# Kernel tuning notes

Hardware: AMD Instinct MI355X
Metric: run time of the kernel (lower is better)

The kernel has to match this reference:

```python
import jax, jax.numpy as jnp
import numpy as np

D = 1024
HEADS = 16
HEAD_DIM = D // HEADS
B = 4
L = 1024


def setup_inputs() -> dict:
    key = jax.random.key(0)
    kq, kk, kv, kw, kb = jax.random.split(key, 5)
    Q = jax.random.normal(kq, (B, L, D), dtype=jnp.float32)
    K = jax.random.normal(kk, (B, L, D), dtype=jnp.float32)
    V = jax.random.normal(kv, (B, L, D), dtype=jnp.float32)
    # Output projection H: torch nn.Linear(D, D) -> weight (D, D), bias (D,)
    lim = 1.0 / np.sqrt(D)
    W_H = jax.random.uniform(kw, (D, D), minval=-lim, maxval=lim, dtype=jnp.float32)
    b_H = jax.random.uniform(kb, (D,), minval=-lim, maxval=lim, dtype=jnp.float32)
    mask = 0  # falsy -> no masking branch, matching `if mask` in the source
    return {"Q": Q, "K": K, "V": V, "W_H": W_H, "b_H": b_H, "mask": mask}


def reference(Q, K, V, W_H, b_H, mask):
    batch, q_len, _ = Q.shape
    k_len = K.shape[1]
    Qh = Q.reshape(batch, q_len, HEADS, HEAD_DIM)
    Kh = K.reshape(batch, k_len, HEADS, HEAD_DIM)
    Vh = V.reshape(batch, k_len, HEADS, HEAD_DIM)
    scores = jnp.einsum('bqhd,bkhd->bhqk', Qh, Kh)  # [B,H,Lq,Lk]
    if mask:  # mask is a Python scalar (0 -> skip), as in source
        scores = jnp.where(mask == 0, -jnp.inf, scores)
    # NOTE: source scales by sqrt(D), not sqrt(head_dim)
    attn = jax.nn.softmax(scores / np.sqrt(D).astype(np.float32), axis=3)
    out = jnp.einsum('bhql,blhd->bqhd', attn, Vh).reshape(batch, q_len, D)
    return out @ W_H.T + b_H
```

## Files before the change

kernel.cpp:

```cpp
#include <hip/hip_runtime.h>
#include <hip/hip_bf16.h>

typedef __attribute__((ext_vector_type(4))) float f32x4;
typedef __attribute__((ext_vector_type(8))) short bf16x8;

constexpr int Bn  = 4;
constexpr int Ln  = 1024;
constexpr int Dn  = 1024;
constexpr int Hn  = 16;
constexpr int HDn = 64;

static __device__ __forceinline__ unsigned short bf16r(float f) {
    union { float f; unsigned int u; } x;
    x.f = f;
    unsigned int r = x.u + 0x7fffu + ((x.u >> 16) & 1u);
    return (unsigned short)(r >> 16);
}

__global__ __launch_bounds__(256) void prep_kernel(
    const float* __restrict__ Kg, const float* __restrict__ Vg,
    const float* __restrict__ Wg, unsigned short* __restrict__ Kbf,
    unsigned short* __restrict__ Vtg, unsigned short* __restrict__ Wbf)
{
    const int tid = threadIdx.x;
    if (blockIdx.z == 4) {
        const int r0 = blockIdx.x * 64, c0 = blockIdx.y * 64;
        for (int i = 0; i < 4; ++i) {
            int e4 = i * 256 + tid;
            int r = e4 >> 4, c4 = e4 & 15;
            const float* p = Wg + (size_t)(r0 + r) * Dn + c0 + c4 * 4;
            float4 v = *(const float4*)p;
            ushort4 o;
            o.x = bf16r(v.x); o.y = bf16r(v.y); o.z = bf16r(v.z); o.w = bf16r(v.w);
            *(ushort4*)(Wbf + (size_t)(r0 + r) * Dn + c0 + c4 * 4) = o;
        }
        return;
    }

    __shared__ unsigned short T[64][72];
    const int k0 = blockIdx.x * 64;
    const int h  = blockIdx.y;
    const int b  = blockIdx.z;
    const float* Kb = Kg + (size_t)b * Ln * Dn + h * HDn;
    const float* Vb = Vg + (size_t)b * Ln * Dn + h * HDn;
    unsigned short* Ko = Kbf + (size_t)b * Ln * Dn + h * HDn;

    for (int i = 0; i < 4; ++i) {
        int e4 = i * 256 + tid;
        int r = e4 >> 4, c4 = e4 & 15;
        float4 kv = *(const float4*)(Kb + (size_t)(k0 + r) * Dn + c4 * 4);
        ushort4 o;
        o.x = bf16r(kv.x); o.y = bf16r(kv.y); o.z = bf16r(kv.z); o.w = bf16r(kv.w);
        *(ushort4*)(Ko + (size_t)(k0 + r) * Dn + c4 * 4) = o;
        float4 vv = *(const float4*)(Vb + (size_t)(k0 + r) * Dn + c4 * 4);
        T[c4 * 4 + 0][r] = bf16r(vv.x);
        T[c4 * 4 + 1][r] = bf16r(vv.y);
        T[c4 * 4 + 2][r] = bf16r(vv.z);
        T[c4 * 4 + 3][r] = bf16r(vv.w);
    }
    __syncthreads();
    unsigned short* out = Vtg + ((size_t)(b * Hn + h) * HDn) * Ln + k0;
    for (int i = 0; i < 2; ++i) {
        int e8 = i * 256 + tid;
        int r = e8 >> 3, c8 = e8 & 7;
        *(uint4*)(out + (size_t)r * Ln + c8 * 8) = *(const uint4*)&T[r][c8 * 8];
    }
}

__global__ __launch_bounds__(512) void attn_kernel(
    const float* __restrict__ Qg, const unsigned short* __restrict__ Kbf,
    const unsigned short* __restrict__ Vtg, unsigned short* __restrict__ Xg)
{
    __shared__ unsigned short Ks[64][72];
    __shared__ unsigned short Vts[64][72];
    __shared__ unsigned short Ps[128][72];

    const int tid  = threadIdx.x;
    const int wave = tid >> 6;
    const int lane = tid & 63;
    const int l16  = lane & 15;
    const int quad = lane >> 4;

    const int q0 = blockIdx.x * 128;
    const int h  = blockIdx.y;
    const int b  = blockIdx.z;

    const unsigned short* Kb16 = Kbf + (size_t)b * Ln * Dn + h * HDn;
    const unsigned short* Vtb  = Vtg + ((size_t)(b * Hn + h) * HDn) * Ln;

    bf16x8 aq0, aq1;
    {
        const float* qp = Qg + ((size_t)b * Ln + q0 + wave * 16 + l16) * Dn
                             + h * HDn + quad * 8;
        float4 a0 = *(const float4*)qp;
        float4 a1 = *(const float4*)(qp + 4);
        float4 a2 = *(const float4*)(qp + 32);
        float4 a3 = *(const float4*)(qp + 36);
        aq0[0] = (short)bf16r(a0.x); aq0[1] = (short)bf16r(a0.y);
        aq0[2] = (short)bf16r(a0.z); aq0[3] = (short)bf16r(a0.w);
        aq0[4] = (short)bf16r(a1.x); aq0[5] = (short)bf16r(a1.y);
        aq0[6] = (short)bf16r(a1.z); aq0[7] = (short)bf16r(a1.w);
        aq1[0] = (short)bf16r(a2.x); aq1[1] = (short)bf16r(a2.y);
        aq1[2] = (short)bf16r(a2.z); aq1[3] = (short)bf16r(a2.w);
        aq1[4] = (short)bf16r(a3.x); aq1[5] = (short)bf16r(a3.y);
        aq1[6] = (short)bf16r(a3.z); aq1[7] = (short)bf16r(a3.w);
    }

    const float SC = 1.4426950408889634f / 32.0f;

    float lsum[4] = {0.f, 0.f, 0.f, 0.f};
    f32x4 Oacc[4];
    for (int d = 0; d < 4; ++d) Oacc[d] = (f32x4){0.f, 0.f, 0.f, 0.f};

    for (int it = 0; it < Ln / 64; ++it) {
        const int k0 = it * 64;
        __syncthreads();
        {
            int r = tid >> 3, c8 = tid & 7;
            *(uint4*)&Ks[r][c8 * 8] =
                *(const uint4*)(Kb16 + (size_t)(k0 + r) * Dn + c8 * 8);
            *(uint4*)&Vts[r][c8 * 8] =
                *(const uint4*)(Vtb + (size_t)r * Ln + k0 + c8 * 8);
        }
        __syncthreads();

        f32x4 s[4];
        for (int n = 0; n < 4; ++n) {
            bf16x8 b0 = *(const bf16x8*)&Ks[n * 16 + l16][quad * 8];
            bf16x8 b1 = *(const bf16x8*)&Ks[n * 16 + l16][32 + quad * 8];
            f32x4 acc = (f32x4){0.f, 0.f, 0.f, 0.f};
            acc = __builtin_amdgcn_mfma_f32_16x16x32_bf16(aq0, b0, acc, 0, 0, 0);
            acc = __builtin_amdgcn_mfma_f32_16x16x32_bf16(aq1, b1, acc, 0, 0, 0);
            s[n] = acc;
        }

        for (int n = 0; n < 4; ++n)
            for (int r = 0; r < 4; ++r) {
                float p = exp2f(s[n][r] * SC);
                s[n][r] = p;
                lsum[r] += p;
            }

        for (int n = 0; n < 4; ++n)
            for (int r = 0; r < 4; ++r)
                Ps[wave * 16 + quad * 4 + r][n * 16 + l16] = bf16r(s[n][r]);

        for (int kk = 0; kk < 2; ++kk) {
            bf16x8 ap = *(const bf16x8*)&Ps[wave * 16 + l16][kk * 32 + quad * 8];
            for (int d = 0; d < 4; ++d) {
                bf16x8 bv = *(const bf16x8*)&Vts[d * 16 + l16][kk * 32 + quad * 8];
                Oacc[d] = __builtin_amdgcn_mfma_f32_16x16x32_bf16(ap, bv, Oacc[d], 0, 0, 0);
            }
        }
    }

    float linv[4];
    for (int r = 0; r < 4; ++r) {
        float rs = lsum[r];
        rs += __shfl_xor(rs, 1, 64);
        rs += __shfl_xor(rs, 2, 64);
        rs += __shfl_xor(rs, 4, 64);
        rs += __shfl_xor(rs, 8, 64);
        linv[r] = 1.f / rs;
    }

    unsigned short* Xb = Xg + ((size_t)b * Ln + q0) * Dn + h * HDn;
    for (int r = 0; r < 4; ++r) {
        int row = wave * 16 + quad * 4 + r;
        for (int d = 0; d < 4; ++d)
            Xb[(size_t)row * Dn + d * 16 + l16] = bf16r(Oacc[d][r] * linv[r]);
    }
}

__global__ __launch_bounds__(256) void proj_kernel(
    const unsigned short* __restrict__ Xg, const unsigned short* __restrict__ Wbf,
    const float* __restrict__ bg, float* __restrict__ Yg)
{
    __shared__ unsigned short Xs[64][136];
    __shared__ unsigned short Wsh[64][136];

    const int tid  = threadIdx.x;
    const int wave = tid >> 6;
    const int lane = tid & 63;
    const int l16  = lane & 15;
    const int quad = lane >> 4;
    const int mw   = (wave & 1) * 32;
    const int nw   = (wave >> 1) * 32;

    const int m0 = blockIdx.x * 64;
    const int n0 = blockIdx.y * 64;

    f32x4 acc[2][2];
    for (int mt = 0; mt < 2; ++mt)
        for (int nt = 0; nt < 2; ++nt)
            acc[mt][nt] = (f32x4){0.f, 0.f, 0.f, 0.f};

    for (int it = 0; it < Dn / 128; ++it) {
        const int kk0 = it * 128;
        __syncthreads();
        for (int i = 0; i < 4; ++i) {
            int idx = i * 256 + tid;
            int r = idx >> 4, c8 = idx & 15;
            *(uint4*)&Xs[r][c8 * 8] =
                *(const uint4*)(Xg + (size_t)(m0 + r) * Dn + kk0 + c8 * 8);
            *(uint4*)&Wsh[r][c8 * 8] =
                *(const uint4*)(Wbf + (size_t)(n0 + r) * Dn + kk0 + c8 * 8);
        }
        __syncthreads();

        for (int kk = 0; kk < 4; ++kk) {
            bf16x8 af[2], bfr[2];
            for (int mt = 0; mt < 2; ++mt)
                af[mt] = *(const bf16x8*)&Xs[mw + mt * 16 + l16][kk * 32 + quad * 8];
            for (int nt = 0; nt < 2; ++nt)
                bfr[nt] = *(const bf16x8*)&Wsh[nw + nt * 16 + l16][kk * 32 + quad * 8];
            for (int mt = 0; mt < 2; ++mt)
                for (int nt = 0; nt < 2; ++nt)
                    acc[mt][nt] = __builtin_amdgcn_mfma_f32_16x16x32_bf16(
                        af[mt], bfr[nt], acc[mt][nt], 0, 0, 0);
        }
    }

    for (int nt = 0; nt < 2; ++nt) {
        int col = n0 + nw + nt * 16 + l16;
        float bb = bg[col];
        for (int mt = 0; mt < 2; ++mt)
            for (int r = 0; r < 4; ++r) {
                int row = m0 + mw + mt * 16 + quad * 4 + r;
                Yg[(size_t)row * Dn + col] = acc[mt][nt][r] + bb;
            }
    }
}

extern "C" void kernel_launch(void* const* d_in, const int* in_sizes, int n_in,
                              void* d_out, int out_size, void* d_ws, size_t ws_size,
                              hipStream_t stream) {
    const float* Q    = (const float*)d_in[0];
    const float* K    = (const float*)d_in[1];
    const float* V    = (const float*)d_in[2];
    const float* W    = (const float*)d_in[3];
    const float* bias = (const float*)d_in[4];

    unsigned short* Kbf = (unsigned short*)d_ws;
    unsigned short* Vt  = Kbf + (size_t)Bn * Ln * Dn;
    unsigned short* Wbf = Vt  + (size_t)Bn * Ln * Dn;
    unsigned short* X   = Wbf + (size_t)Dn * Dn;
    float* Y = (float*)d_out;

    dim3 gp(Ln / 64, Hn, Bn + 1);
    prep_kernel<<<gp, 256, 0, stream>>>(K, V, W, Kbf, Vt, Wbf);

    dim3 g1(Ln / 128, Hn, Bn);
    attn_kernel<<<g1, 512, 0, stream>>>(Q, Kbf, Vt, X);

    dim3 g2((Bn * Ln) / 64, Dn / 64);
    proj_kernel<<<g2, 256, 0, stream>>>(X, Wbf, bias, Y);
}
```

Baseline: 157.5 us.

## Widen attention tile to 256 queries, prefetch K/V, swizzle blocks per XCD

Each wave now handles 32 query rows instead of 16, so every K/V tile loaded from shared memory feeds twice as many MFMAs. The score MFMA operands are swapped, which produces S transposed, and P is written to shared memory with packed 8-byte stores. The next K/V tile is prefetched into registers before the compute of the current one, overlapping global loads with math. Blocks are remapped so that all query tiles of the same (batch, head) land on one XCD for L2 reuse. In exchange the grid drops to 256 blocks, which halves parallelism, and register pressure rises.

```diff
diff --git a/kernel.cpp b/kernel.cpp
--- a/kernel.cpp
+++ b/kernel.cpp
@@ -15,6 +15,10 @@
     x.f = f;
     unsigned int r = x.u + 0x7fffu + ((x.u >> 16) & 1u);
     return (unsigned short)(r >> 16);
+}
+
+static __device__ __forceinline__ unsigned int pk2(float a, float b) {
+    return (unsigned int)bf16r(a) | ((unsigned int)bf16r(b) << 16);
 }
 
 __global__ __launch_bounds__(256) void prep_kernel(
@@ -73,103 +77,128 @@
 {
     __shared__ unsigned short Ks[64][72];
     __shared__ unsigned short Vts[64][72];
-    __shared__ unsigned short Ps[128][72];
+    __shared__ unsigned short Ps[256][72];
 
     const int tid  = threadIdx.x;
     const int wave = tid >> 6;
     const int lane = tid & 63;
     const int l16  = lane & 15;
     const int quad = lane >> 4;
-
-    const int q0 = blockIdx.x * 128;
-    const int h  = blockIdx.y;
-    const int b  = blockIdx.z;
+    const int wb   = wave * 32;
+
+    const int flat = blockIdx.x;
+    const int xcd  = flat & 7;
+    const int j    = flat >> 3;
+    const int qt   = j & 3;
+    const int gg   = j >> 2;
+    const int g    = xcd + 8 * gg;
+    const int h    = g & 15;
+    const int b    = g >> 4;
+    const int q0   = qt * 256;
 
     const unsigned short* Kb16 = Kbf + (size_t)b * Ln * Dn + h * HDn;
     const unsigned short* Vtb  = Vtg + ((size_t)(b * Hn + h) * HDn) * Ln;
 
-    bf16x8 aq0, aq1;
-    {
-        const float* qp = Qg + ((size_t)b * Ln + q0 + wave * 16 + l16) * Dn
+    bf16x8 bq[2][2];
+    for (int hf = 0; hf < 2; ++hf) {
+        const float* qp = Qg + ((size_t)b * Ln + q0 + wb + hf * 16 + l16) * Dn
                              + h * HDn + quad * 8;
         float4 a0 = *(const float4*)qp;
         float4 a1 = *(const float4*)(qp + 4);
         float4 a2 = *(const float4*)(qp + 32);
         float4 a3 = *(const float4*)(qp + 36);
-        aq0[0] = (short)bf16r(a0.x); aq0[1] = (short)bf16r(a0.y);
-        aq0[2] = (short)bf16r(a0.z); aq0[3] = (short)bf16r(a0.w);
-        aq0[4] = (short)bf16r(a1.x); aq0[5] = (short)bf16r(a1.y);
-        aq0[6] = (short)bf16r(a1.z); aq0[7] = (short)bf16r(a1.w);
-        aq1[0] = (short)bf16r(a2.x); aq1[1] = (short)bf16r(a2.y);
-        aq1[2] = (short)bf16r(a2.z); aq1[3] = (short)bf16r(a2.w);
-        aq1[4] = (short)bf16r(a3.x); aq1[5] = (short)bf16r(a3.y);
-        aq1[6] = (short)bf16r(a3.z); aq1[7] = (short)bf16r(a3.w);
+        bq[hf][0][0] = (short)bf16r(a0.x); bq[hf][0][1] = (short)bf16r(a0.y);
+        bq[hf][0][2] = (short)bf16r(a0.z); bq[hf][0][3] = (short)bf16r(a0.w);
+        bq[hf][0][4] = (short)bf16r(a1.x); bq[hf][0][5] = (short)bf16r(a1.y);
+        bq[hf][0][6] = (short)bf16r(a1.z); bq[hf][0][7] = (short)bf16r(a1.w);
+        bq[hf][1][0] = (short)bf16r(a2.x); bq[hf][1][1] = (short)bf16r(a2.y);
+        bq[hf][1][2] = (short)bf16r(a2.z); bq[hf][1][3] = (short)bf16r(a2.w);
+        bq[hf][1][4] = (short)bf16r(a3.x); bq[hf][1][5] = (short)bf16r(a3.y);
+        bq[hf][1][6] = (short)bf16r(a3.z); bq[hf][1][7] = (short)bf16r(a3.w);
     }
 
     const float SC = 1.4426950408889634f / 32.0f;
 
-    float lsum[4] = {0.f, 0.f, 0.f, 0.f};
-    f32x4 Oacc[4];
-    for (int d = 0; d < 4; ++d) Oacc[d] = (f32x4){0.f, 0.f, 0.f, 0.f};
+    float lsum[2] = {0.f, 0.f};
+    f32x4 Oacc[2][4];
+    for (int hf = 0; hf < 2; ++hf)
+        for (int d = 0; d < 4; ++d) Oacc[hf][d] = (f32x4){0.f, 0.f, 0.f, 0.f};
+
+    const int sr = tid >> 3, sc = tid & 7;
+    uint4 kreg, vreg;
+    {
+        kreg = *(const uint4*)(Kb16 + (size_t)sr * Dn + sc * 8);
+        vreg = *(const uint4*)(Vtb + (size_t)sr * Ln + sc * 8);
+    }
 
     for (int it = 0; it < Ln / 64; ++it) {
-        const int k0 = it * 64;
-        __syncthreads();
-        {
-            int r = tid >> 3, c8 = tid & 7;
-            *(uint4*)&Ks[r][c8 * 8] =
-                *(const uint4*)(Kb16 + (size_t)(k0 + r) * Dn + c8 * 8);
-            *(uint4*)&Vts[r][c8 * 8] =
-                *(const uint4*)(Vtb + (size_t)r * Ln + k0 + c8 * 8);
-        }
-        __syncthreads();
-
-        f32x4 s[4];
+        __syncthreads();
+        *(uint4*)&Ks[sr][sc * 8]  = kreg;
+        *(uint4*)&Vts[sr][sc * 8] = vreg;
+        if (it + 1 < Ln / 64) {
+            const int k1 = (it + 1) * 64;
+            kreg = *(const uint4*)(Kb16 + (size_t)(k1 + sr) * Dn + sc * 8);
+            vreg = *(const uint4*)(Vtb + (size_t)sr * Ln + k1 + sc * 8);
+        }
+        __syncthreads();
+
+        f32x4 st[2][4];
         for (int n = 0; n < 4; ++n) {
-            bf16x8 b0 = *(const bf16x8*)&Ks[n * 16 + l16][quad * 8];
-            bf16x8 b1 = *(const bf16x8*)&Ks[n * 16 + l16][32 + quad * 8];
-            f32x4 acc = (f32x4){0.f, 0.f, 0.f, 0.f};
-            acc = __builtin_amdgcn_mfma_f32_16x16x32_bf16(aq0, b0, acc, 0, 0, 0);
-            acc = __builtin_amdgcn_mfma_f32_16x16x32_bf16(aq1, b1, acc, 0, 0, 0);
-            s[n] = acc;
-        }
-
-        for (int n = 0; n < 4; ++n)
-            for (int r = 0; r < 4; ++r) {
-                float p = exp2f(s[n][r] * SC);
-                s[n][r] = p;
-                lsum[r] += p;
-            }
-
-        for (int n = 0; n < 4; ++n)
-            for (int r = 0; r < 4; ++r)
-                Ps[wave * 16 + quad * 4 + r][n * 16 + l16] = bf16r(s[n][r]);
+            bf16x8 a0 = *(const bf16x8*)&Ks[n * 16 + l16][quad * 8];
+            bf16x8 a1 = *(const bf16x8*)&Ks[n * 16 + l16][32 + quad * 8];
+            for (int hf = 0; hf < 2; ++hf) {
+                f32x4 acc = (f32x4){0.f, 0.f, 0.f, 0.f};
+                acc = __builtin_amdgcn_mfma_f32_16x16x32_bf16(a0, bq[hf][0], acc, 0, 0, 0);
+                acc = __builtin_amdgcn_mfma_f32_16x16x32_bf16(a1, bq[hf][1], acc, 0, 0, 0);
+                st[hf][n] = acc;
+            }
+        }
+
+        for (int hf = 0; hf < 2; ++hf) {
+            float ls = 0.f;
+            for (int n = 0; n < 4; ++n) {
+                float p0 = exp2f(st[hf][n][0] * SC);
+                float p1 = exp2f(st[hf][n][1] * SC);
+                float p2 = exp2f(st[hf][n][2] * SC);
+                float p3 = exp2f(st[hf][n][3] * SC);
+                ls += (p0 + p1) + (p2 + p3);
+                uint2 w;
+                w.x = pk2(p0, p1);
+                w.y = pk2(p2, p3);
+                *(uint2*)&Ps[wb + hf * 16 + l16][n * 16 + quad * 4] = w;
+            }
+            lsum[hf] += ls;
+        }
 
         for (int kk = 0; kk < 2; ++kk) {
-            bf16x8 ap = *(const bf16x8*)&Ps[wave * 16 + l16][kk * 32 + quad * 8];
-            for (int d = 0; d < 4; ++d) {
-                bf16x8 bv = *(const bf16x8*)&Vts[d * 16 + l16][kk * 32 + quad * 8];
-                Oacc[d] = __builtin_amdgcn_mfma_f32_16x16x32_bf16(ap, bv, Oacc[d], 0, 0, 0);
-            }
-        }
-    }
-
-    float linv[4];
-    for (int r = 0; r < 4; ++r) {
-        float rs = lsum[r];
-        rs += __shfl_xor(rs, 1, 64);
-        rs += __shfl_xor(rs, 2, 64);
-        rs += __shfl_xor(rs, 4, 64);
-        rs += __shfl_xor(rs, 8, 64);
-        linv[r] = 1.f / rs;
-    }
-
-    unsigned short* Xb = Xg + ((size_t)b * Ln + q0) * Dn + h * HDn;
-    for (int r = 0; r < 4; ++r) {
-        int row = wave * 16 + quad * 4 + r;
-        for (int d = 0; d < 4; ++d)
-            Xb[(size_t)row * Dn + d * 16 + l16] = bf16r(Oacc[d][r] * linv[r]);
-    }
+            bf16x8 bv[4];
+            for (int dt = 0; dt < 4; ++dt)
+                bv[dt] = *(const bf16x8*)&Vts[dt * 16 + l16][kk * 32 + quad * 8];
+            for (int hf = 0; hf < 2; ++hf) {
+                bf16x8 ap = *(const bf16x8*)&Ps[wb + hf * 16 + l16][kk * 32 + quad * 8];
+                for (int dt = 0; dt < 4; ++dt)
+                    Oacc[hf][dt] = __builtin_amdgcn_mfma_f32_16x16x32_bf16(
+                        ap, bv[dt], Oacc[hf][dt], 0, 0, 0);
+            }
+        }
+    }
+
+    float inv[2];
+    for (int hf = 0; hf < 2; ++hf) {
+        float rs = lsum[hf];
+        rs += __shfl_xor(rs, 16, 64);
+        rs += __shfl_xor(rs, 32, 64);
+        inv[hf] = 1.f / rs;
+    }
+
+    unsigned short* Xb = Xg + ((size_t)b * Ln + q0 + wb) * Dn + h * HDn;
+    for (int hf = 0; hf < 2; ++hf)
+        for (int r = 0; r < 4; ++r) {
+            float iv = __shfl(inv[hf], quad * 4 + r, 64);
+            int row = hf * 16 + quad * 4 + r;
+            for (int dt = 0; dt < 4; ++dt)
+                Xb[(size_t)row * Dn + dt * 16 + l16] = bf16r(Oacc[hf][dt][r] * iv);
+        }
 }
 
 __global__ __launch_bounds__(256) void proj_kernel(
@@ -250,8 +279,7 @@
     dim3 gp(Ln / 64, Hn, Bn + 1);
     prep_kernel<<<gp, 256, 0, stream>>>(K, V, W, Kbf, Vt, Wbf);
 
-    dim3 g1(Ln / 128, Hn, Bn);
-    attn_kernel<<<g1, 512, 0, stream>>>(Q, Kbf, Vt, X);
+    attn_kernel<<<dim3(256, 1, 1), 512, 0, stream>>>(Q, Kbf, Vt, X);
 
     dim3 g2((Bn * Ln) / 64, Dn / 64);
     proj_kernel<<<g2, 256, 0, stream>>>(X, Wbf, bias, Y);
```

Result: slower. 212.6 us (+35.0%).
